# Kernel optimization log

Measured on AMD Instinct MI355X. Metric: run time of the kernel, lower is better.

The kernel has to match this reference:

```python
import jax, jax.numpy as jnp
import numpy as np

B, H, LK, D = 8, 16, 4096, 128


def setup_inputs() -> dict:
    key = jax.random.key(0)
    ks = jax.random.split(key, 9)
    s = 1.0 / np.sqrt(D)
    return {
        "Q": jax.random.normal(ks[0], (B, H, 1, D), dtype=jnp.float32),
        "K": jax.random.normal(ks[1], (B, H, LK, D), dtype=jnp.float32),
        "V": jax.random.normal(ks[2], (B, H, LK, D), dtype=jnp.float32),
        "mask": jax.random.randint(ks[3], (B, H, 1, LK), 0, 2, dtype=jnp.int32),
        "scale": 1,  # accepted but unused by the original forward
        "W_pre": jax.random.normal(ks[4], (D, D), dtype=jnp.float32) * s,
        "b_pre": jax.random.normal(ks[5], (D,), dtype=jnp.float32) * s,
        "W_q": jax.random.normal(ks[6], (D, D), dtype=jnp.float32) * s,
        "W_v": jax.random.normal(ks[7], (D, 1), dtype=jnp.float32) * s,
    }


def reference(Q, K, V, mask, scale, W_pre, b_pre, W_q, W_v):
    # precompute = linear_pre(K): [B,H,LK,D]
    pre = jnp.einsum("bhkd,de->bhke", K, W_pre) + b_pre
    # targetT = linear_q(Q): [B,H,1,D], broadcast-added over keys
    tq = jnp.einsum("bhqd,de->bhqe", Q, W_q)
    tmp = jnp.tanh(pre + tq)  # [B,H,LK,D]
    # energy = linear_v(tmp) reshaped to [B,H,1,LK]
    energy = jnp.einsum("bhkd,d->bhk", tmp, W_v[:, 0])[:, :, None, :]
    m = mask.astype(energy.dtype)
    energy = energy * (1.0 - m) + m * (-1e6)
    score = jax.nn.softmax(energy, axis=-1)  # [B,H,1,LK]
    context = jnp.matmul(score, V)  # [B,H,1,D]
    return (context, score, pre)
```

## Files before the change

### kernel.cpp

```cpp
#include <hip/hip_runtime.h>
#include <hip/hip_bf16.h>
#include <math.h>

#define B_   8
#define H_   16
#define BH_  (B_*H_)
#define LK_  4096
#define D_   128

#define SEG   16
#define KSEG  (LK_/SEG)

typedef __attribute__((ext_vector_type(8))) short bf16x8;
typedef __attribute__((ext_vector_type(4))) float f32x4;
typedef __attribute__((ext_vector_type(4))) unsigned int u32x4;

__device__ __forceinline__ float fast_tanh(float x) {
    float ax = fabsf(x);
    float e  = __expf(2.0f * ax);
    float r  = 1.0f - __fdividef(2.0f, e + 1.0f);
    return copysignf(r, x);
}

__device__ __forceinline__ unsigned int cvtpk(float lo, float hi) {
    unsigned int r;
    asm("v_cvt_pk_bf16_f32 %0, %1, %2" : "=v"(r) : "v"(lo), "v"(hi));
    return r;
}

__device__ __forceinline__ unsigned short cvt_hi(float x) {
    __hip_bfloat16 bh = __float2bfloat16(x);
    return __builtin_bit_cast(unsigned short, bh);
}

__device__ __forceinline__ void cvt8v(const f32x4 a, const f32x4 b, bf16x8& h, bf16x8& l) {
    unsigned int h0 = cvtpk(a[0], a[1]);
    unsigned int h1 = cvtpk(a[2], a[3]);
    unsigned int h2 = cvtpk(b[0], b[1]);
    unsigned int h3 = cvtpk(b[2], b[3]);
    float l0 = a[0] - __uint_as_float(h0 << 16);
    float l1 = a[1] - __uint_as_float(h0 & 0xFFFF0000u);
    float l2 = a[2] - __uint_as_float(h1 << 16);
    float l3 = a[3] - __uint_as_float(h1 & 0xFFFF0000u);
    float l4 = b[0] - __uint_as_float(h2 << 16);
    float l5 = b[1] - __uint_as_float(h2 & 0xFFFF0000u);
    float l6 = b[2] - __uint_as_float(h3 << 16);
    float l7 = b[3] - __uint_as_float(h3 & 0xFFFF0000u);
    u32x4 hv = {h0, h1, h2, h3};
    u32x4 lv = {cvtpk(l0, l1), cvtpk(l2, l3), cvtpk(l4, l5), cvtpk(l6, l7)};
    h = __builtin_bit_cast(bf16x8, hv);
    l = __builtin_bit_cast(bf16x8, lv);
}

__device__ __forceinline__ void gld_lds16(const void* g, void* l) {
    __builtin_amdgcn_global_load_lds(
        (const __attribute__((address_space(1))) unsigned int*)g,
        (__attribute__((address_space(3))) unsigned int*)l,
        16, 0, 0);
}

__global__ void pack_kernel(const float* __restrict__ Wpre,
                            unsigned short* __restrict__ Whi) {
    int idx  = blockIdx.x * 256 + threadIdx.x;
    int j    = idx & 7;
    int lane = (idx >> 3) & 63;
    int nt   = (idx >> 9) & 7;
    int ks   = idx >> 12;
    int k    = ks * 32 + (lane >> 4) * 8 + j;
    int n    = nt * 16 + (lane & 15);
    Whi[idx] = cvt_hi(Wpre[k * D_ + n]);
}

__global__ void tq_kernel(const float* __restrict__ Q,
                          const float* __restrict__ Wq,
                          float* __restrict__ tq) {
    int bh = blockIdx.x;
    int e  = threadIdx.x;
    const float* q = Q + bh * D_;
    float acc = 0.0f;
#pragma unroll 8
    for (int d = 0; d < D_; ++d)
        acc = fmaf(q[d], Wq[d * D_ + e], acc);
    tq[bh * D_ + e] = acc;
}

__global__ void __launch_bounds__(256, 2)
main_kernel(const float* __restrict__ K,
            const unsigned short* __restrict__ Whi,
            const float* __restrict__ bpre,
            const float* __restrict__ Wv,
            const float* __restrict__ tqg,
            float* __restrict__ pre_out,
            float* __restrict__ ep0,
            float* __restrict__ ep1) {
    const int t    = threadIdx.x;
    const int lane = t & 63;
    const int wv_  = t >> 6;
    const int kg   = wv_ & 1;
    const int eh   = wv_ >> 1;
    const int l15  = lane & 15;
    const int lg   = lane >> 4;
    const int bh   = blockIdx.y;
    const int kblk = blockIdx.x * 256;

    __shared__ float Klds[4][4096];

    const float* Kbh = K + (size_t)bh * LK_ * D_;

    bf16x8 wf[4][4];
#pragma unroll
    for (int ks = 0; ks < 4; ++ks)
#pragma unroll
        for (int et = 0; et < 4; ++et)
            wf[ks][et] = *(const bf16x8*)(Whi + (((size_t)ks * 8 + eh * 4 + et) * 64 + lane) * 8);

    float4 bpv[4], tqv[4], wvv[4];
#pragma unroll
    for (int et = 0; et < 4; ++et) {
        const int e0 = eh * 64 + et * 16 + lg * 4;
        bpv[et] = *(const float4*)(bpre + e0);
        tqv[et] = *(const float4*)(tqg + bh * D_ + e0);
        wvv[et] = *(const float4*)(Wv + e0);
    }

    float* epo = (eh == 0) ? ep0 : ep1;

    auto stageK = [&](int s, int buf) {
#pragma unroll
        for (int i = 0; i < 4; ++i) {
            const int g4  = wv_ * 4 + i;
            const int kg2 = g4 >> 3, ks2 = (g4 >> 1) & 3, h2 = g4 & 1;
            const int row = kblk + s * 32 + kg2 * 16 + l15;
            const int col = lg * 8 + ks2 * 32 + h2 * 4;
            gld_lds16(Kbh + (size_t)row * D_ + col, &Klds[buf][g4 * 256]);
        }
    };

    stageK(0, 0);
    stageK(1, 1);
    stageK(2, 2);
    asm volatile("s_waitcnt vmcnt(8)\n\ts_barrier" ::: "memory");

#pragma unroll
    for (int s = 0; s < 8; ++s) {
        if (s + 3 < 8) stageK(s + 3, (s + 3) & 3);

        const float* kb = Klds[s & 3];
        f32x4 acc[4];
#pragma unroll
        for (int et = 0; et < 4; ++et)
            acc[et] = (f32x4){0.f, 0.f, 0.f, 0.f};

#pragma unroll
        for (int ks = 0; ks < 4; ++ks) {
            const int gbase = ((kg * 4 + ks) * 2) * 256 + lane * 4;
            f32x4 p0 = *(const f32x4*)(kb + gbase);
            f32x4 p1 = *(const f32x4*)(kb + gbase + 256);
            bf16x8 kh, kl;
            cvt8v(p0, p1, kh, kl);
#pragma unroll
            for (int et = 0; et < 4; ++et) {
                acc[et] = __builtin_amdgcn_mfma_f32_16x16x32_bf16(wf[ks][et], kh, acc[et], 0, 0, 0);
                acc[et] = __builtin_amdgcn_mfma_f32_16x16x32_bf16(wf[ks][et], kl, acc[et], 0, 0, 0);
            }
        }

        const int key = kblk + s * 32 + kg * 16 + l15;
        float* pb = pre_out + (size_t)bh * LK_ * D_ + (size_t)key * D_;
        float ep = 0.0f;
#pragma unroll
        for (int et = 0; et < 4; ++et) {
            const int e0 = eh * 64 + et * 16 + lg * 4;
            f32x4 a = acc[et];
            f32x4 v;
            v[0] = a[0] + bpv[et].x;
            v[1] = a[1] + bpv[et].y;
            v[2] = a[2] + bpv[et].z;
            v[3] = a[3] + bpv[et].w;
            *(f32x4*)(pb + e0) = v;
            ep = fmaf(fast_tanh(v[0] + tqv[et].x), wvv[et].x, ep);
            ep = fmaf(fast_tanh(v[1] + tqv[et].y), wvv[et].y, ep);
            ep = fmaf(fast_tanh(v[2] + tqv[et].z), wvv[et].z, ep);
            ep = fmaf(fast_tanh(v[3] + tqv[et].w), wvv[et].w, ep);
        }
        ep += __shfl_xor(ep, 16, 64);
        ep += __shfl_xor(ep, 32, 64);
        epo[(size_t)bh * LK_ + key] = ep;

        if (s == 0)
            asm volatile("s_waitcnt vmcnt(13)\n\ts_barrier" ::: "memory");
        else if (s == 1)
            asm volatile("s_waitcnt vmcnt(18)\n\ts_barrier" ::: "memory");
        else if (s < 5)
            asm volatile("s_waitcnt vmcnt(23)\n\ts_barrier" ::: "memory");
        else if (s == 5)
            asm volatile("s_waitcnt vmcnt(19)\n\ts_barrier" ::: "memory");
        else if (s == 6)
            asm volatile("s_waitcnt vmcnt(15)\n\ts_barrier" ::: "memory");
    }
}

__global__ void ml_kernel(const float* __restrict__ ep0,
                          const float* __restrict__ ep1,
                          const int* __restrict__ mask,
                          float* __restrict__ ml) {
    const int bh = blockIdx.x;
    const int t  = threadIdx.x;
    const float* e0 = ep0 + (size_t)bh * LK_;
    const float* e1 = ep1 + (size_t)bh * LK_;
    const int*   m  = mask + (size_t)bh * LK_;

    float mx = -1e30f;
    for (int k = t; k < LK_; k += 256) {
        float v = m[k] ? -1.0e6f : (e0[k] + e1[k]);
        mx = fmaxf(mx, v);
    }
#pragma unroll
    for (int off = 32; off > 0; off >>= 1)
        mx = fmaxf(mx, __shfl_xor(mx, off, 64));
    __shared__ float wmax[4];
    if ((t & 63) == 0) wmax[t >> 6] = mx;
    __syncthreads();
    mx = fmaxf(fmaxf(wmax[0], wmax[1]), fmaxf(wmax[2], wmax[3]));

    float sum = 0.0f;
    for (int k = t; k < LK_; k += 256) {
        float v = m[k] ? -1.0e6f : (e0[k] + e1[k]);
        sum += __expf(v - mx);
    }
#pragma unroll
    for (int off = 32; off > 0; off >>= 1)
        sum += __shfl_xor(sum, off, 64);
    __shared__ float wsum[4];
    if ((t & 63) == 0) wsum[t >> 6] = sum;
    __syncthreads();
    if (t == 0) {
        ml[bh * 2]     = mx;
        ml[bh * 2 + 1] = wsum[0] + wsum[1] + wsum[2] + wsum[3];
    }
}

__global__ void score_ctx_kernel(const float* __restrict__ ep1,
                                 const int* __restrict__ mask,
                                 const float* __restrict__ V,
                                 const float* __restrict__ ml,
                                 float* __restrict__ score_out,
                                 float* __restrict__ part) {
    const int seg = blockIdx.x;
    const int bh  = blockIdx.y;
    const int t   = threadIdx.x;
    const int k0  = seg * KSEG;

    __shared__ float sc[KSEG];
    __shared__ float pl[8][136];

    const float mx  = ml[bh * 2];
    const float inv = 1.0f / ml[bh * 2 + 1];

    {
        const size_t gi = (size_t)bh * LK_ + k0 + t;
        float v = mask[gi] ? -1.0e6f : (score_out[gi] + ep1[gi]);
        float s = __expf(v - mx) * inv;
        sc[t] = s;
        score_out[gi] = s;
    }
    __syncthreads();

    const int d4 = t & 31;
    const int g  = t >> 5;
    const float* Vb = V + ((size_t)bh * LK_ + k0) * D_ + d4 * 4;
    float4 a = make_float4(0.f, 0.f, 0.f, 0.f);
#pragma unroll 4
    for (int kk = g; kk < KSEG; kk += 8) {
        float4 vv = *(const float4*)(Vb + (size_t)kk * D_);
        float s = sc[kk];
        a.x = fmaf(s, vv.x, a.x);
        a.y = fmaf(s, vv.y, a.y);
        a.z = fmaf(s, vv.z, a.z);
        a.w = fmaf(s, vv.w, a.w);
    }
    *(float4*)&pl[g][d4 * 4] = a;
    __syncthreads();

    if (t < 128) {
        float s = 0.0f;
#pragma unroll
        for (int gg = 0; gg < 8; ++gg)
            s += pl[gg][t];
        part[((size_t)bh * SEG + seg) * D_ + t] = s;
    }
}

__global__ void combine_kernel(const float* __restrict__ part,
                               float* __restrict__ ctx) {
    const int bh = blockIdx.x;
    const int d  = threadIdx.x;
    float s = 0.0f;
#pragma unroll
    for (int g = 0; g < SEG; ++g)
        s += part[((size_t)bh * SEG + g) * D_ + d];
    ctx[bh * D_ + d] = s;
}

extern "C" void kernel_launch(void* const* d_in, const int* in_sizes, int n_in,
                              void* d_out, int out_size, void* d_ws, size_t ws_size,
                              hipStream_t stream) {
    const float* Q    = (const float*)d_in[0];
    const float* K    = (const float*)d_in[1];
    const float* V    = (const float*)d_in[2];
    const int*   mask = (const int*)  d_in[3];
    const float* Wpre = (const float*)d_in[5];
    const float* bpre = (const float*)d_in[6];
    const float* Wq   = (const float*)d_in[7];
    const float* Wv   = (const float*)d_in[8];

    float* out   = (float*)d_out;
    float* ctx   = out;
    float* score = out + (size_t)BH_ * D_;
    float* pre   = score + (size_t)BH_ * LK_;

    float* w    = (float*)d_ws;
    float* tq   = w;
    float* ml   = tq + (size_t)BH_ * D_;
    float* part = ml + 2 * BH_;
    unsigned short* Whi = (unsigned short*)(part + (size_t)BH_ * SEG * D_);
    float* ep1  = (float*)(Whi + 16384);

    hipLaunchKernelGGL(pack_kernel, dim3(64), dim3(256), 0, stream, Wpre, Whi);
    hipLaunchKernelGGL(tq_kernel, dim3(BH_), dim3(D_), 0, stream, Q, Wq, tq);
    hipLaunchKernelGGL(main_kernel, dim3(LK_ / 256, BH_), dim3(256), 0, stream,
                       K, Whi, bpre, Wv, tq, pre, score, ep1);
    hipLaunchKernelGGL(ml_kernel, dim3(BH_), dim3(256), 0, stream, score, ep1, mask, ml);
    hipLaunchKernelGGL(score_ctx_kernel, dim3(SEG, BH_), dim3(256), 0, stream,
                       ep1, mask, V, ml, score, part);
    hipLaunchKernelGGL(combine_kernel, dim3(BH_), dim3(D_), 0, stream, part, ctx);
}
```

Measured before the change: 219.6 us.

## Split main kernel into single-wave blocks per output half with 4-deep pipeline

Each main_kernel block becomes a single 64-lane wavefront that handles one half of the output columns over 256 keys, in 16 steps of 16 keys. A 4-buffer LDS ring is used and the prefetch is issued after the MFMA loop. Because only one wave touches LDS, the s_barrier calls are removed and only vmcnt waits remain. The cost is that each of the two output-half blocks now loads the full K rows, so K reads from global memory double, in exchange for less barrier synchronisation and more independent blocks.

```diff
diff --git a/kernel.cpp b/kernel.cpp
--- a/kernel.cpp
+++ b/kernel.cpp
@@ -84,7 +84,7 @@
     tq[bh * D_ + e] = acc;
 }
 
-__global__ void __launch_bounds__(256, 2)
+__global__ void __launch_bounds__(64)
 main_kernel(const float* __restrict__ K,
             const unsigned short* __restrict__ Whi,
             const float* __restrict__ bpre,
@@ -93,17 +93,14 @@
             float* __restrict__ pre_out,
             float* __restrict__ ep0,
             float* __restrict__ ep1) {
-    const int t    = threadIdx.x;
-    const int lane = t & 63;
-    const int wv_  = t >> 6;
-    const int kg   = wv_ & 1;
-    const int eh   = wv_ >> 1;
+    const int lane = threadIdx.x;
     const int l15  = lane & 15;
     const int lg   = lane >> 4;
-    const int bh   = blockIdx.y;
+    const int eh   = blockIdx.y;
+    const int bh   = blockIdx.z;
     const int kblk = blockIdx.x * 256;
 
-    __shared__ float Klds[4][4096];
+    __shared__ float Klds[4][2048];
 
     const float* Kbh = K + (size_t)bh * LK_ * D_;
 
@@ -127,10 +124,9 @@
 
     auto stageK = [&](int s, int buf) {
 #pragma unroll
-        for (int i = 0; i < 4; ++i) {
-            const int g4  = wv_ * 4 + i;
-            const int kg2 = g4 >> 3, ks2 = (g4 >> 1) & 3, h2 = g4 & 1;
-            const int row = kblk + s * 32 + kg2 * 16 + l15;
+        for (int g4 = 0; g4 < 8; ++g4) {
+            const int ks2 = g4 >> 1, h2 = g4 & 1;
+            const int row = kblk + s * 16 + l15;
             const int col = lg * 8 + ks2 * 32 + h2 * 4;
             gld_lds16(Kbh + (size_t)row * D_ + col, &Klds[buf][g4 * 256]);
         }
@@ -139,12 +135,11 @@
     stageK(0, 0);
     stageK(1, 1);
     stageK(2, 2);
-    asm volatile("s_waitcnt vmcnt(8)\n\ts_barrier" ::: "memory");
-
-#pragma unroll
-    for (int s = 0; s < 8; ++s) {
-        if (s + 3 < 8) stageK(s + 3, (s + 3) & 3);
-
+    stageK(3, 3);
+    asm volatile("s_waitcnt vmcnt(24)" ::: "memory");
+
+#pragma unroll
+    for (int s = 0; s < 16; ++s) {
         const float* kb = Klds[s & 3];
         f32x4 acc[4];
 #pragma unroll
@@ -153,9 +148,8 @@
 
 #pragma unroll
         for (int ks = 0; ks < 4; ++ks) {
-            const int gbase = ((kg * 4 + ks) * 2) * 256 + lane * 4;
-            f32x4 p0 = *(const f32x4*)(kb + gbase);
-            f32x4 p1 = *(const f32x4*)(kb + gbase + 256);
+            f32x4 p0 = *(const f32x4*)(kb + (ks * 2) * 256 + lane * 4);
+            f32x4 p1 = *(const f32x4*)(kb + (ks * 2 + 1) * 256 + lane * 4);
             bf16x8 kh, kl;
             cvt8v(p0, p1, kh, kl);
 #pragma unroll
@@ -165,7 +159,9 @@
             }
         }
 
-        const int key = kblk + s * 32 + kg * 16 + l15;
+        if (s + 4 < 16) stageK(s + 4, (s + 4) & 3);
+
+        const int key = kblk + s * 16 + l15;
         float* pb = pre_out + (size_t)bh * LK_ * D_ + (size_t)key * D_;
         float ep = 0.0f;
 #pragma unroll
@@ -188,15 +184,19 @@
         epo[(size_t)bh * LK_ + key] = ep;
 
         if (s == 0)
-            asm volatile("s_waitcnt vmcnt(13)\n\ts_barrier" ::: "memory");
+            asm volatile("s_waitcnt vmcnt(29)" ::: "memory");
         else if (s == 1)
-            asm volatile("s_waitcnt vmcnt(18)\n\ts_barrier" ::: "memory");
-        else if (s < 5)
-            asm volatile("s_waitcnt vmcnt(23)\n\ts_barrier" ::: "memory");
-        else if (s == 5)
-            asm volatile("s_waitcnt vmcnt(19)\n\ts_barrier" ::: "memory");
-        else if (s == 6)
-            asm volatile("s_waitcnt vmcnt(15)\n\ts_barrier" ::: "memory");
+            asm volatile("s_waitcnt vmcnt(34)" ::: "memory");
+        else if (s == 2)
+            asm volatile("s_waitcnt vmcnt(39)" ::: "memory");
+        else if (s <= 11)
+            asm volatile("s_waitcnt vmcnt(44)" ::: "memory");
+        else if (s == 12)
+            asm volatile("s_waitcnt vmcnt(36)" ::: "memory");
+        else if (s == 13)
+            asm volatile("s_waitcnt vmcnt(28)" ::: "memory");
+        else if (s == 14)
+            asm volatile("s_waitcnt vmcnt(20)" ::: "memory");
     }
 }
 
@@ -328,7 +328,7 @@
 
     hipLaunchKernelGGL(pack_kernel, dim3(64), dim3(256), 0, stream, Wpre, Whi);
     hipLaunchKernelGGL(tq_kernel, dim3(BH_), dim3(D_), 0, stream, Q, Wq, tq);
-    hipLaunchKernelGGL(main_kernel, dim3(LK_ / 256, BH_), dim3(256), 0, stream,
+    hipLaunchKernelGGL(main_kernel, dim3(LK_ / 256, 2, BH_), dim3(64), 0, stream,
                        K, Whi, bpre, Wv, tq, pre, score, ep1);
     hipLaunchKernelGGL(ml_kernel, dim3(BH_), dim3(256), 0, stream, score, ep1, mask, ml);
     hipLaunchKernelGGL(score_ctx_kernel, dim3(SEG, BH_), dim3(256), 0, stream,
```

New measurement: 249.4 us. 13.6% more time.
